# Optimization experiments

Measured on AMD Instinct MI355X. Metric: run time of the kernel, lower is better.

The kernel has to match this reference:

```python
import jax, jax.numpy as jnp
import numpy as np
from jax import lax

B, T, I, H = 4096, 512, 1, 32

def setup_inputs() -> dict:
    key = jax.random.key(0)
    ks = jax.random.split(key, 7)
    s = 1.0 / np.sqrt(H)
    return {
        "x": jax.random.normal(ks[0], (B, T, I), dtype=jnp.float32),
        "W_ih": jax.random.uniform(ks[1], (4 * H, I), minval=-s, maxval=s, dtype=jnp.float32),
        "W_hh": jax.random.uniform(ks[2], (4 * H, H), minval=-s, maxval=s, dtype=jnp.float32),
        "b_ih": jax.random.uniform(ks[3], (4 * H,), minval=-s, maxval=s, dtype=jnp.float32),
        "b_hh": jax.random.uniform(ks[4], (4 * H,), minval=-s, maxval=s, dtype=jnp.float32),
        "W_lin": jax.random.uniform(ks[5], (1, H), minval=-s, maxval=s, dtype=jnp.float32),
        "b_lin": jax.random.uniform(ks[6], (1,), minval=-s, maxval=s, dtype=jnp.float32),
    }

def reference(x, W_ih, W_hh, b_ih, b_hh, W_lin, b_lin):
    b, t, _ = x.shape
    h = W_hh.shape[1]
    # Precompute input contribution to all gates for all timesteps: [T,B,4H]
    xg = jnp.einsum('bti,gi->tbg', x, W_ih) + b_ih + b_hh

    def step(carry, xt):
        hs, cs = carry
        g = xt + hs @ W_hh.T  # [B,4H], PyTorch gate order i,f,g,o
        i = jax.nn.sigmoid(g[:, :h])
        f = jax.nn.sigmoid(g[:, h:2 * h])
        gg = jnp.tanh(g[:, 2 * h:3 * h])
        o = jax.nn.sigmoid(g[:, 3 * h:])
        cs = f * cs + i * gg
        hs = o * jnp.tanh(cs)
        return (hs, cs), None

    h0 = jnp.zeros((b, h), dtype=x.dtype)
    c0 = jnp.zeros((b, h), dtype=x.dtype)
    (h_last, _), _ = lax.scan(step, (h0, c0), xg)
    # final linear on last hidden state: [B,1]
    return h_last @ W_lin.T + b_lin
```

## Files before the change

kernel.cpp:

```cpp
#include <hip/hip_runtime.h>


typedef float f32x4 __attribute__((ext_vector_type(4)));
typedef _Float16 f16x8 __attribute__((ext_vector_type(8)));

#define L2E 1.44269504088896340736f
#define MFMA16(a, b, c) __builtin_amdgcn_mfma_f32_16x16x32_f16((a), (b), (c), 0, 0, 0)

union H2U { _Float16 h; unsigned short u; };
union FRAG { int i[4]; f16x8 h; };

__device__ __forceinline__ float sig_pre(float t) {
    return __builtin_amdgcn_rcpf(1.0f + __builtin_amdgcn_exp2f(t));
}
__device__ __forceinline__ float tanh_pre(float t) {
    return fmaf(__builtin_amdgcn_rcpf(1.0f + __builtin_amdgcn_exp2f(t)), 2.0f, -1.0f);
}

__global__ __launch_bounds__(256, 1) void lstm_mfma_kernel(
    const float* __restrict__ x,
    const float* __restrict__ W_ih,
    const float* __restrict__ W_hh,
    const float* __restrict__ b_ih,
    const float* __restrict__ b_hh,
    const float* __restrict__ W_lin,
    const float* __restrict__ b_lin,
    float* __restrict__ out,
    int B)
{
    const int tid  = (int)threadIdx.x;
    const int wid  = tid >> 6;
    const int lane = tid & 63;
    const int col  = lane & 15;
    const int g    = lane >> 4;

    int bidx[4];
#pragma unroll
    for (int j = 0; j < 4; ++j) bidx[j] = ((4 * g + j) + 16 * (col >> 2)) << 2;

    f16x8 bf[8];
    float wihs[8];
    f32x4 biasC[8];
#pragma unroll
    for (int t = 0; t < 8; ++t) {
        const int gr = t * 16 + col;
        const float sc = (t == 4 || t == 5) ? (-2.0f * L2E) : (-L2E);
        const float* wr = &W_hh[gr * 32];
        f16x8 bb;
#pragma unroll
        for (int j = 0; j < 4; ++j) {
            bb[2 * j + 0] = (_Float16)(wr[4 * g + j] * sc);
            bb[2 * j + 1] = (_Float16)(wr[16 + 4 * g + j] * sc);
        }
        bf[t] = bb;
        wihs[t] = W_ih[gr] * sc;
        const float bbias = (b_ih[gr] + b_hh[gr]) * sc;
        biasC[t] = f32x4{bbias, 0.0f, 0.0f, 0.0f};
    }

    const int b_glob = blockIdx.x * 16 + wid * 4 + g;
    const int bc     = b_glob < B ? b_glob : (B - 1);
    const float* xb  = x + (size_t)bc * 512;

    float4 xA = *reinterpret_cast<const float4*>(xb);
    float4 xB = *reinterpret_cast<const float4*>(xb + 4);

    float cc0 = 0.0f, cc1 = 0.0f, h0 = 0.0f, h1 = 0.0f;

    for (int tc = 0; tc < 64; ++tc) {
        const int nbase = ((tc + 1) & 63) * 8;
        const float4 nA = *reinterpret_cast<const float4*>(xb + nbase);
        const float4 nB = *reinterpret_cast<const float4*>(xb + nbase + 4);
        const float xts[8] = {xA.x, xA.y, xA.z, xA.w, xB.x, xB.y, xB.z, xB.w};

#pragma unroll
        for (int s = 0; s < 8; ++s) {
            const float xt = xts[s];

            H2U p0, p1; p0.h = (_Float16)h0; p1.h = (_Float16)h1;
            const int hu = (int)((unsigned)p0.u | ((unsigned)p1.u << 16));

            FRAG fr;
#pragma unroll
            for (int j = 0; j < 4; ++j)
                fr.i[j] = __builtin_amdgcn_ds_bpermute(bidx[j], hu);

            f32x4 acc[8];
#pragma unroll
            for (int t = 0; t < 8; ++t) acc[t] = MFMA16(fr.h, bf[t], biasC[t]);

            float gt[8];
#pragma unroll
            for (int t = 0; t < 8; ++t) gt[t] = fmaf(xt, wihs[t], acc[t][0]);

            const float i0 = sig_pre(gt[0]),  i1 = sig_pre(gt[1]);
            const float f0 = sig_pre(gt[2]),  f1 = sig_pre(gt[3]);
            const float G0 = tanh_pre(gt[4]), G1 = tanh_pre(gt[5]);
            const float o0 = sig_pre(gt[6]),  o1 = sig_pre(gt[7]);

            cc0 = fmaf(f0, cc0, i0 * G0);
            cc1 = fmaf(f1, cc1, i1 * G1);
            h0 = o0 * tanh_pre(cc0 * (-2.0f * L2E));
            h1 = o1 * tanh_pre(cc1 * (-2.0f * L2E));
        }
        xA = nA; xB = nB;
    }

    float part = h0 * W_lin[col] + h1 * W_lin[col + 16];
    part += __shfl_xor(part, 1, 64);
    part += __shfl_xor(part, 2, 64);
    part += __shfl_xor(part, 4, 64);
    part += __shfl_xor(part, 8, 64);
    if (col == 0 && b_glob < B) out[b_glob] = part + b_lin[0];
}

extern "C" void kernel_launch(void* const* d_in, const int* in_sizes, int n_in,
                              void* d_out, int out_size, void* d_ws, size_t ws_size,
                              hipStream_t stream) {
    const float* x     = (const float*)d_in[0];
    const float* W_ih  = (const float*)d_in[1];
    const float* W_hh  = (const float*)d_in[2];
    const float* b_ih  = (const float*)d_in[3];
    const float* b_hh  = (const float*)d_in[4];
    const float* W_lin = (const float*)d_in[5];
    const float* b_lin = (const float*)d_in[6];
    float* out = (float*)d_out;

    const int B = in_sizes[0] / 512;
    const int blocks = (B + 15) / 16;

    lstm_mfma_kernel<<<blocks, 256, 0, stream>>>(x, W_ih, W_hh, b_ih, b_hh,
                                                 W_lin, b_lin, out, B);
}
```

Before: 131.8 us.

## Halve batch per wave and spread gate nonlinearities across lanes via permlane32 swap

Each wave now processes 2 batch rows instead of 4. The MFMA output rows holding the two gate halves are merged across lanes with permlane32_swap, so every lane evaluates one cell's four gates rather than eight, which shortens the serial transcendental chain per timestep. The new hidden value is repacked with another permlane swap plus a byte perm. The launch grows to twice as many blocks and the min-occupancy launch bound is dropped, trading MFMA utilization (half the rows wasted) for a shorter per-step critical path and more waves in flight.

```diff
diff --git a/kernel.cpp b/kernel.cpp
--- a/kernel.cpp
+++ b/kernel.cpp
@@ -3,12 +3,14 @@
 
 typedef float f32x4 __attribute__((ext_vector_type(4)));
 typedef _Float16 f16x8 __attribute__((ext_vector_type(8)));
+typedef unsigned int v2u __attribute__((ext_vector_type(2)));
 
 #define L2E 1.44269504088896340736f
 #define MFMA16(a, b, c) __builtin_amdgcn_mfma_f32_16x16x32_f16((a), (b), (c), 0, 0, 0)
 
 union H2U { _Float16 h; unsigned short u; };
 union FRAG { int i[4]; f16x8 h; };
+union F2U { float f; unsigned u; };
 
 __device__ __forceinline__ float sig_pre(float t) {
     return __builtin_amdgcn_rcpf(1.0f + __builtin_amdgcn_exp2f(t));
@@ -17,7 +19,14 @@
     return fmaf(__builtin_amdgcn_rcpf(1.0f + __builtin_amdgcn_exp2f(t)), 2.0f, -1.0f);
 }
 
-__global__ __launch_bounds__(256, 1) void lstm_mfma_kernel(
+__device__ __forceinline__ float merge_gates(float even, float odd) {
+    F2U a, b; a.f = even; b.f = odd;
+    v2u r = __builtin_amdgcn_permlane32_swap(a.u, b.u, false, false);
+    F2U o; o.u = r.x;
+    return o.f;
+}
+
+__global__ __launch_bounds__(256) void lstm_mfma_kernel(
     const float* __restrict__ x,
     const float* __restrict__ W_ih,
     const float* __restrict__ W_hh,
@@ -29,17 +38,16 @@
     int B)
 {
     const int tid  = (int)threadIdx.x;
-    const int wid  = tid >> 6;
+    const int wv   = tid >> 6;
     const int lane = tid & 63;
     const int col  = lane & 15;
     const int g    = lane >> 4;
 
     int bidx[4];
 #pragma unroll
-    for (int j = 0; j < 4; ++j) bidx[j] = ((4 * g + j) + 16 * (col >> 2)) << 2;
+    for (int j = 0; j < 4; ++j) bidx[j] = (16 * (col >> 2) + 4 * g + j) << 2;
 
     f16x8 bf[8];
-    float wihs[8];
     f32x4 biasC[8];
 #pragma unroll
     for (int t = 0; t < 8; ++t) {
@@ -53,65 +61,87 @@
             bb[2 * j + 1] = (_Float16)(wr[16 + 4 * g + j] * sc);
         }
         bf[t] = bb;
-        wihs[t] = W_ih[gr] * sc;
         const float bbias = (b_ih[gr] + b_hh[gr]) * sc;
         biasC[t] = f32x4{bbias, 0.0f, 0.0f, 0.0f};
     }
 
-    const int b_glob = blockIdx.x * 16 + wid * 4 + g;
-    const int bc     = b_glob < B ? b_glob : (B - 1);
-    const float* xb  = x + (size_t)bc * 512;
+    const int cell = col + 16 * (g >> 1);
+    const float wI = W_ih[cell]      * (-L2E);
+    const float wF = W_ih[32 + cell] * (-L2E);
+    const float wG = W_ih[64 + cell] * (-2.0f * L2E);
+    const float wO = W_ih[96 + cell] * (-L2E);
+    const bool useQ = (g & 1) != 0;
 
-    float4 xA = *reinterpret_cast<const float4*>(xb);
-    float4 xB = *reinterpret_cast<const float4*>(xb + 4);
+    const int bP  = blockIdx.x * 8 + wv * 2;
+    const int bQ  = bP + 1;
+    const int bPc = bP < B ? bP : (B - 1);
+    const int bQc = bQ < B ? bQ : (B - 1);
+    const float* xbP = x + (size_t)bPc * 512;
+    const float* xbQ = x + (size_t)bQc * 512;
 
-    float cc0 = 0.0f, cc1 = 0.0f, h0 = 0.0f, h1 = 0.0f;
+    float4 xAP = *reinterpret_cast<const float4*>(xbP);
+    float4 xBP = *reinterpret_cast<const float4*>(xbP + 4);
+    float4 xAQ = *reinterpret_cast<const float4*>(xbQ);
+    float4 xBQ = *reinterpret_cast<const float4*>(xbQ + 4);
+
+    float cc = 0.0f, hh = 0.0f;
+    unsigned hu = 0u;
 
     for (int tc = 0; tc < 64; ++tc) {
         const int nbase = ((tc + 1) & 63) * 8;
-        const float4 nA = *reinterpret_cast<const float4*>(xb + nbase);
-        const float4 nB = *reinterpret_cast<const float4*>(xb + nbase + 4);
-        const float xts[8] = {xA.x, xA.y, xA.z, xA.w, xB.x, xB.y, xB.z, xB.w};
+        const float4 nAP = *reinterpret_cast<const float4*>(xbP + nbase);
+        const float4 nBP = *reinterpret_cast<const float4*>(xbP + nbase + 4);
+        const float4 nAQ = *reinterpret_cast<const float4*>(xbQ + nbase);
+        const float4 nBQ = *reinterpret_cast<const float4*>(xbQ + nbase + 4);
+        const float xtsP[8] = {xAP.x, xAP.y, xAP.z, xAP.w, xBP.x, xBP.y, xBP.z, xBP.w};
+        const float xtsQ[8] = {xAQ.x, xAQ.y, xAQ.z, xAQ.w, xBQ.x, xBQ.y, xBQ.z, xBQ.w};
 
 #pragma unroll
         for (int s = 0; s < 8; ++s) {
-            const float xt = xts[s];
-
-            H2U p0, p1; p0.h = (_Float16)h0; p1.h = (_Float16)h1;
-            const int hu = (int)((unsigned)p0.u | ((unsigned)p1.u << 16));
-
             FRAG fr;
 #pragma unroll
             for (int j = 0; j < 4; ++j)
-                fr.i[j] = __builtin_amdgcn_ds_bpermute(bidx[j], hu);
+                fr.i[j] = __builtin_amdgcn_ds_bpermute(bidx[j], (int)hu);
 
             f32x4 acc[8];
 #pragma unroll
             for (int t = 0; t < 8; ++t) acc[t] = MFMA16(fr.h, bf[t], biasC[t]);
 
-            float gt[8];
-#pragma unroll
-            for (int t = 0; t < 8; ++t) gt[t] = fmaf(xt, wihs[t], acc[t][0]);
+            float gi = merge_gates(acc[0][0], acc[1][0]);
+            float gf = merge_gates(acc[2][0], acc[3][0]);
+            float gG = merge_gates(acc[4][0], acc[5][0]);
+            float go = merge_gates(acc[6][0], acc[7][0]);
 
-            const float i0 = sig_pre(gt[0]),  i1 = sig_pre(gt[1]);
-            const float f0 = sig_pre(gt[2]),  f1 = sig_pre(gt[3]);
-            const float G0 = tanh_pre(gt[4]), G1 = tanh_pre(gt[5]);
-            const float o0 = sig_pre(gt[6]),  o1 = sig_pre(gt[7]);
+            const float xt = useQ ? xtsQ[s] : xtsP[s];
+            gi = fmaf(xt, wI, gi);
+            gf = fmaf(xt, wF, gf);
+            gG = fmaf(xt, wG, gG);
+            go = fmaf(xt, wO, go);
 
-            cc0 = fmaf(f0, cc0, i0 * G0);
-            cc1 = fmaf(f1, cc1, i1 * G1);
-            h0 = o0 * tanh_pre(cc0 * (-2.0f * L2E));
-            h1 = o1 * tanh_pre(cc1 * (-2.0f * L2E));
+            const float i_ = sig_pre(gi);
+            const float f_ = sig_pre(gf);
+            const float G_ = tanh_pre(gG);
+            const float o_ = sig_pre(go);
+
+            cc = fmaf(f_, cc, i_ * G_);
+            hh = o_ * tanh_pre(cc * (-2.0f * L2E));
+
+            H2U hc; hc.h = (_Float16)hh;
+            v2u rr = __builtin_amdgcn_permlane32_swap((unsigned)hc.u, (unsigned)hc.u,
+                                                      false, false);
+            hu = __builtin_amdgcn_perm(rr.y, rr.x, 0x05040100u);
         }
-        xA = nA; xB = nB;
+        xAP = nAP; xBP = nBP; xAQ = nAQ; xBQ = nBQ;
     }
 
-    float part = h0 * W_lin[col] + h1 * W_lin[col + 16];
+    float part = hh * W_lin[cell];
     part += __shfl_xor(part, 1, 64);
     part += __shfl_xor(part, 2, 64);
     part += __shfl_xor(part, 4, 64);
     part += __shfl_xor(part, 8, 64);
-    if (col == 0 && b_glob < B) out[b_glob] = part + b_lin[0];
+    part += __shfl_xor(part, 32, 64);
+    if (col == 0 && g == 0 && bP < B) out[bP] = part + b_lin[0];
+    if (col == 0 && g == 1 && bQ < B) out[bQ] = part + b_lin[0];
 }
 
 extern "C" void kernel_launch(void* const* d_in, const int* in_sizes, int n_in,
@@ -127,7 +157,7 @@
     float* out = (float*)d_out;
 
     const int B = in_sizes[0] / 512;
-    const int blocks = (B + 15) / 16;
+    const int blocks = (B + 7) / 8;
 
     lstm_mfma_kernel<<<blocks, 256, 0, stream>>>(x, W_ih, W_hh, b_ih, b_hh,
                                                  W_lin, b_lin, out, B);
```

Measured after the change: 170.7 us. +29.6%, slower.
